# Kernel optimization log

Hardware: AMD Instinct MI355X
Metric: run time of the kernel (lower is better)

The kernel has to match this reference:

```python
import jax, jax.numpy as jnp
import numpy as np

B, N, H, D = 4, 2048, 8, 64
DM = 512  # model dim = H * D


def setup_inputs() -> dict:
    key = jax.random.key(0)
    ks = jax.random.split(key, 8)
    x = jax.random.normal(ks[0], (B, N, DM), dtype=jnp.float32)
    mask_k = jax.random.randint(ks[1], (B, N), 0, 5) > 0
    mask_q = jax.random.randint(ks[2], (B, N), 0, 5) > 0
    s_in = 1.0 / np.sqrt(DM)
    s_out = 1.0 / np.sqrt(H * D)
    Wq = jax.random.normal(ks[3], (DM, H * D), dtype=jnp.float32) * s_in
    Wk = jax.random.normal(ks[4], (DM, H * D), dtype=jnp.float32) * s_in
    Wv = jax.random.normal(ks[5], (DM, H * D), dtype=jnp.float32) * s_in
    Wo = jax.random.normal(ks[6], (H * D, DM), dtype=jnp.float32) * s_out
    bo = jnp.zeros((DM,), dtype=jnp.float32)
    return {"x": x, "Wq": Wq, "Wk": Wk, "Wv": Wv, "Wo": Wo, "bo": bo,
            "mask_k": mask_k, "mask_q": mask_q}


def reference(x, Wq, Wk, Wv, Wo, bo, mask_k, mask_q):
    b, n, _ = x.shape
    # projections (no bias), split into heads: b n (h d) -> b n h d
    q = (x @ Wq).reshape(b, n, H, D)
    k = (x @ Wk).reshape(b, n, H, D)
    v = (x @ Wv).reshape(b, n, H, D)
    scale = D ** (-0.5)
    sim = jnp.einsum('bihd,bjhd->bijh', q, k) * scale  # [b, i, j, h]
    big_neg = jnp.finfo(jnp.float32).min
    sim = jnp.where(mask_k[:, None, :, None], sim, big_neg)
    sim = jnp.where(mask_q[:, :, None, None], sim, big_neg)
    attn = jax.nn.softmax(sim, axis=-2)  # softmax over key axis j
    out = jnp.einsum('bijh,bjhd->bihd', attn, v).reshape(b, n, H * D)
    return out @ Wo + bo
```

## Files before the change

### kernel.cpp

```cpp
#include <hip/hip_runtime.h>

typedef _Float16 f16;
typedef __fp16   fp16x2 __attribute__((ext_vector_type(2)));
typedef _Float16 f16x8 __attribute__((ext_vector_type(8)));
typedef float    f32x4 __attribute__((ext_vector_type(4)));

#define MFMA16(A, B, C) __builtin_amdgcn_mfma_f32_16x16x32_f16((A), (B), (C), 0, 0, 0)

__device__ __forceinline__ void gl_lds16(const void* g, void* l) {
  __builtin_amdgcn_global_load_lds(
      (const __attribute__((address_space(1))) void*)g,
      (__attribute__((address_space(3))) void*)l, 16, 0, 0);
}

static constexpr size_t OFF_XH  = 0;
static constexpr size_t OFF_WQT = 8388608;
static constexpr size_t OFF_WOT = OFF_WQT + 3 * 524288;
static constexpr size_t OFF_QH  = OFF_WOT + 524288;
static constexpr size_t OFF_KH  = OFF_QH + 8388608;
static constexpr size_t OFF_VT  = OFF_KH + 8388608;
static constexpr size_t OFF_A2  = OFF_VT + 8388608;
static constexpr size_t OFF_AMK = OFF_A2 + 8388608;
static constexpr size_t OFF_VM  = OFF_AMK + 32768;

#define QSCALE 0.18033688011112042f
#define NEGFIX -11.541560327111708f

__global__ void k_cvt_x(const float* __restrict__ x, f16* __restrict__ xh,
                        const int* __restrict__ mask_k, float* __restrict__ amk) {
  int i = blockIdx.x * blockDim.x + threadIdx.x;
  const float4* p = (const float4*)x + (size_t)i * 2;
  float4 a = p[0], b = p[1];
  f16x8 o = { (f16)a.x, (f16)a.y, (f16)a.z, (f16)a.w,
              (f16)b.x, (f16)b.y, (f16)b.z, (f16)b.w };
  *((f16x8*)xh + i) = o;
  if (i < 8192) amk[i] = mask_k[i] ? 0.0f : -1000.0f;
}

__global__ void k_cvt_w4(const float* __restrict__ w0, const float* __restrict__ w1,
                         const float* __restrict__ w2, const float* __restrict__ w3,
                         f16* __restrict__ dst) {
  __shared__ float tile[32][33];
  const int z = blockIdx.z;
  const float* w = (z == 0) ? w0 : (z == 1) ? w1 : (z == 2) ? w2 : w3;
  const float sc = (z == 0) ? QSCALE : 1.0f;
  f16* wt = dst + (size_t)z * 262144;
  int tx = threadIdx.x & 31, ty = threadIdx.x >> 5;
  int bx = blockIdx.x, by = blockIdx.y;
#pragma unroll
  for (int i = 0; i < 32; i += 8)
    tile[ty + i][tx] = w[(size_t)(by * 32 + ty + i) * 512 + bx * 32 + tx];
  __syncthreads();
#pragma unroll
  for (int i = 0; i < 32; i += 8)
    wt[(size_t)(bx * 32 + ty + i) * 512 + by * 32 + tx] = (f16)(tile[tx][ty + i] * sc);
}

__global__ void k_vmean(const f16* __restrict__ Vt, float* __restrict__ vm) {
  int row = blockIdx.x * 4 + (threadIdx.x >> 6);
  int lane = threadIdx.x & 63;
  const f16x8* p = (const f16x8*)(Vt + (size_t)row * 2048) + lane;
  float s = 0.f;
#pragma unroll
  for (int i = 0; i < 4; ++i) {
    f16x8 v = p[i * 64];
#pragma unroll
    for (int e = 0; e < 8; ++e) s += (float)v[e];
  }
#pragma unroll
  for (int i = 32; i; i >>= 1) s += __shfl_xor(s, i, 64);
  if (lane == 0) vm[row] = s * (1.0f / 2048.0f);
}

template <int MODE, int BM, int BN>
__global__ __launch_bounds__(256, (MODE == 2 ? 3 : 2))
void k_gemm(const f16* __restrict__ A, const f16* __restrict__ Bt,
            void* __restrict__ O0, void* __restrict__ O1, void* __restrict__ O2,
            const float* __restrict__ bias) {
  constexpr int MR = BM / 32, NF = BN / 32;
  constexpr int AP = BM / 32, BP = BN / 32;
  constexpr int ABYTES = BM * 128;
  constexpr int BBYTES = BN * 128;
  constexpr int SM_STAGE  = 2 * (ABYTES + BBYTES);
  constexpr int SM_BOUNCE = (MODE == 3) ? 128 * 136 * 2 : 0;
  constexpr int SM = SM_STAGE > SM_BOUNCE ? SM_STAGE : SM_BOUNCE;
  __shared__ __align__(16) char smem[SM];
  const int t = threadIdx.x;
  const int lane = t & 63, w = t >> 6;
  const int wr = w >> 1, wc = w & 1;
  const int l15 = lane & 15, l4 = lane >> 4;
  const int lr = lane >> 3, lc = lane & 7;
  const int flat = blockIdx.x + gridDim.x * blockIdx.y;
  const int nwg  = gridDim.x * gridDim.y;
  const int sw   = (flat & 7) * (nwg >> 3) + (flat >> 3);
  const int row0 = (sw / gridDim.x) * BM;
  const int col0 = (sw % gridDim.x) * BN;

  f32x4 acc[MR][NF] = {};

  auto stage = [&](int kt, int buf) {
    char* dA = smem + buf * ABYTES + w * 1024;
    char* dB = smem + 2 * ABYTES + buf * BBYTES + w * 1024;
#pragma unroll
    for (int p = 0; p < AP; ++p) {
      int r = p * 32 + w * 8 + lr;
      gl_lds16((const char*)A + ((size_t)(row0 + r) * 512 + kt) * 2 + ((lc ^ (r & 7)) << 4),
               dA + p * 4096);
    }
#pragma unroll
    for (int p = 0; p < BP; ++p) {
      int r = p * 32 + w * 8 + lr;
      gl_lds16((const char*)Bt + ((size_t)(col0 + r) * 512 + kt) * 2 + ((lc ^ (r & 7)) << 4),
               dB + p * 4096);
    }
  };

  stage(0, 0);
  for (int ks = 0; ks < 8; ++ks) {
    const int buf = ks & 1;
    __syncthreads();
    if (ks < 7) stage((ks + 1) * 64, buf ^ 1);
    const char* cA = smem + buf * ABYTES;
    const char* cB = smem + 2 * ABYTES + buf * BBYTES;
    __builtin_amdgcn_s_setprio(1);
#pragma unroll
    for (int kb = 0; kb < 2; ++kb) {
      f16x8 af[MR], bf[NF];
#pragma unroll
      for (int m = 0; m < MR; ++m) {
        int r = wr * (BM / 2) + m * 16 + l15;
        int lb = r * 128 + kb * 64 + l4 * 16;
        af[m] = *(const f16x8*)(cA + (lb ^ ((r & 7) << 4)));
      }
#pragma unroll
      for (int n = 0; n < NF; ++n) {
        int r = wc * (BN / 2) + n * 16 + l15;
        int lb = r * 128 + kb * 64 + l4 * 16;
        bf[n] = *(const f16x8*)(cB + (lb ^ ((r & 7) << 4)));
      }
#pragma unroll
      for (int m = 0; m < MR; ++m)
#pragma unroll
        for (int n = 0; n < NF; ++n)
          acc[m][n] = MFMA16(af[m], bf[n], acc[m][n]);
    }
    __builtin_amdgcn_s_setprio(0);
  }

  if (MODE == 2) {
#pragma unroll
    for (int m = 0; m < MR; ++m)
#pragma unroll
      for (int n = 0; n < NF; ++n) {
        int gr = row0 + wr * (BM / 2) + m * 16 + l4 * 4;
        int gc = col0 + wc * (BN / 2) + n * 16 + l15;
        float* C = (float*)O0;
        float bv = bias[gc];
#pragma unroll
        for (int rr = 0; rr < 4; ++rr)
          C[(size_t)(gr + rr) * 512 + gc] = acc[m][n][rr] + bv;
      }
  } else {
    int seg = col0 >> 9;
    if (seg < 2) {
      __syncthreads();
      f16* bb = (f16*)smem;
#pragma unroll
      for (int m = 0; m < MR; ++m)
#pragma unroll
        for (int n = 0; n < NF; ++n) {
          int r = wr * (BM / 2) + m * 16 + l4 * 4;
          int c = wc * (BN / 2) + n * 16 + l15;
#pragma unroll
          for (int rr = 0; rr < 4; ++rr)
            bb[(r + rr) * 136 + c] = (f16)acc[m][n][rr];
        }
      __syncthreads();
      f16* C = (f16*)(seg == 0 ? O0 : O1);
      int cbase = col0 & 511;
#pragma unroll
      for (int i = 0; i < 8; ++i) {
        int idx = i * 256 + t;
        int r = idx >> 4, c8 = (idx & 15) * 8;
        uint4 v = *(const uint4*)(bb + r * 136 + c8);
        *(uint4*)(C + (size_t)(row0 + r) * 512 + cbase + c8) = v;
      }
    } else {
#pragma unroll
      for (int m = 0; m < MR; ++m)
#pragma unroll
        for (int n = 0; n < NF; ++n) {
          int gr = row0 + wr * (BM / 2) + m * 16 + l4 * 4;
          int lcol = (col0 & 511) + wc * (BN / 2) + n * 16 + l15;
          f16* C = (f16*)O2;
          int hh = lcol >> 6, dd = lcol & 63;
          int bb2 = gr >> 11, ns = gr & 2047;
          union { uint2 u2; f16 v[4]; } pk;
#pragma unroll
          for (int rr = 0; rr < 4; ++rr) pk.v[rr] = (f16)acc[m][n][rr];
          *(uint2*)(C + (size_t)((bb2 * 8 + hh) * 64 + dd) * 2048 + ns) = pk.u2;
        }
    }
  }
}

__global__ __launch_bounds__(256, 3)
void k_attn(const f16* __restrict__ Q, const f16* __restrict__ K,
            const f16* __restrict__ Vt, const float* __restrict__ amk,
            const int* __restrict__ mask_q, const float* __restrict__ vmean,
            f16* __restrict__ A2) {
  __shared__ __align__(16) f16 sK[2][64 * 64];
  __shared__ __align__(16) f16 sV[2][64 * 64];
  __shared__ __align__(16) f16 sP[4][32 * 64];
  const int t = threadIdx.x, lane = t & 63, w = t >> 6;
  const int l15 = lane & 15, l4 = lane >> 4;
  const int lr = lane >> 3, lc = lane & 7;
  const int sw = (blockIdx.x & 7) * 64 + (blockIdx.x >> 3);
  const int qx = sw & 15, bh = sw >> 4;
  const int b = bh >> 3, h = bh & 7;
  const int q0 = qx * 128 + w * 32;

  f16x8 qa[2][2];
#pragma unroll
  for (int g = 0; g < 2; ++g) {
    const f16* qb = Q + (size_t)(b * 2048 + q0 + g * 16 + l15) * 512 + h * 64 + l4 * 8;
    qa[g][0] = *(const f16x8*)qb;
    qa[g][1] = *(const f16x8*)(qb + 32);
  }

  const f16x8 onesv = { (f16)1.f, (f16)1.f, (f16)1.f, (f16)1.f,
                        (f16)1.f, (f16)1.f, (f16)1.f, (f16)1.f };
  f32x4 o[2][4] = {};
  f32x4 oex[2] = {};

  const char* Kbase  = (const char*)K + ((size_t)b * 2048 * 512 + h * 64) * 2;
  const char* VtBase = (const char*)Vt + ((size_t)(b * 8 + h) * 64) * 2048 * 2;
  const float* amkb = amk + b * 2048;
  char* sPw = (char*)&sP[w][0];

  auto stage = [&](int kv, int buf) {
#pragma unroll
    for (int p = 0; p < 2; ++p) {
      int r = p * 32 + w * 8 + lr;
      gl_lds16(Kbase + (size_t)(kv + r) * 1024 + ((lc ^ (r & 7)) << 4),
               (char*)&sK[buf][0] + p * 4096 + w * 1024);
    }
#pragma unroll
    for (int p = 0; p < 2; ++p) {
      int d = p * 32 + w * 8 + lr;
      gl_lds16(VtBase + ((size_t)d * 2048 + kv) * 2 + ((lc ^ (d & 7)) << 4),
               (char*)&sV[buf][0] + p * 4096 + w * 1024);
    }
  };

  stage(0, 0);
  for (int it = 0; it < 32; ++it) {
    const int kv = it * 64, buf = it & 1;
    __syncthreads();
    if (it < 31) stage(kv + 64, buf ^ 1);
    const char* cK = (const char*)&sK[buf][0];
    const char* cV = (const char*)&sV[buf][0];

    f32x4 amv[4];
#pragma unroll
    for (int jf = 0; jf < 4; ++jf)
      amv[jf] = *(const f32x4*)(amkb + kv + jf * 16 + l4 * 4);

    f32x4 sT[2][4];
    __builtin_amdgcn_s_setprio(1);
#pragma unroll
    for (int jf = 0; jf < 4; ++jf) {
      int r = jf * 16 + l15;
      int base = r * 128 + l4 * 16;
      f16x8 k0 = *(const f16x8*)(cK + (base ^ ((r & 7) << 4)));
      f16x8 k1 = *(const f16x8*)(cK + ((base + 64) ^ ((r & 7) << 4)));
#pragma unroll
      for (int g = 0; g < 2; ++g) {
        f32x4 z = { NEGFIX, NEGFIX, NEGFIX, NEGFIX };
        z = MFMA16(k0, qa[g][0], z);
        z = MFMA16(k1, qa[g][1], z);
        sT[g][jf] = z;
      }
    }
    __builtin_amdgcn_s_setprio(0);

#pragma unroll
    for (int g = 0; g < 2; ++g)
#pragma unroll
      for (int jf = 0; jf < 4; ++jf) {
        float p0 = __builtin_amdgcn_exp2f(sT[g][jf][0] + amv[jf][0]);
        float p1 = __builtin_amdgcn_exp2f(sT[g][jf][1] + amv[jf][1]);
        float p2 = __builtin_amdgcn_exp2f(sT[g][jf][2] + amv[jf][2]);
        float p3 = __builtin_amdgcn_exp2f(sT[g][jf][3] + amv[jf][3]);
        fp16x2 a01 = __builtin_amdgcn_cvt_pkrtz(p0, p1);
        fp16x2 a23 = __builtin_amdgcn_cvt_pkrtz(p2, p3);
        uint2 pk = { __builtin_bit_cast(unsigned, a01),
                     __builtin_bit_cast(unsigned, a23) };
        int row = g * 16 + l15;
        int boff = row * 128 + jf * 32 + l4 * 8;
        *(uint2*)(sPw + (boff ^ ((row & 7) << 4))) = pk;
      }

    __builtin_amdgcn_s_setprio(1);
#pragma unroll
    for (int kb = 0; kb < 2; ++kb) {
      f16x8 pa[2];
#pragma unroll
      for (int g = 0; g < 2; ++g) {
        int rq = g * 16 + l15;
        int pbase = rq * 128 + kb * 64 + l4 * 16;
        pa[g] = *(const f16x8*)(sPw + (pbase ^ ((rq & 7) << 4)));
        oex[g] = MFMA16(pa[g], onesv, oex[g]);
      }
#pragma unroll
      for (int df = 0; df < 4; ++df) {
        int d = df * 16 + l15;
        int vbase = d * 128 + kb * 64 + l4 * 16;
        f16x8 bv = *(const f16x8*)(cV + (vbase ^ ((d & 7) << 4)));
#pragma unroll
        for (int g = 0; g < 2; ++g)
          o[g][df] = MFMA16(pa[g], bv, o[g][df]);
      }
    }
    __builtin_amdgcn_s_setprio(0);
  }

#pragma unroll
  for (int g = 0; g < 2; ++g) {
    const int4 mq4 = *(const int4*)(mask_q + b * 2048 + q0 + g * 16 + l4 * 4);
    const int mq[4] = { mq4.x, mq4.y, mq4.z, mq4.w };
    float inv[4];
#pragma unroll
    for (int rr = 0; rr < 4; ++rr) inv[rr] = 1.0f / oex[g][rr];
#pragma unroll
    for (int df = 0; df < 4; ++df) {
      float vm = vmean[(b * 8 + h) * 64 + df * 16 + l15];
#pragma unroll
      for (int rr = 0; rr < 4; ++rr) {
        float val = mq[rr] ? (o[g][df][rr] * inv[rr]) : vm;
        A2[(size_t)(b * 2048 + q0 + g * 16 + l4 * 4 + rr) * 512 + h * 64 + df * 16 + l15] =
            (f16)val;
      }
    }
  }
}

extern "C" void kernel_launch(void* const* d_in, const int* in_sizes, int n_in,
                              void* d_out, int out_size, void* d_ws, size_t ws_size,
                              hipStream_t stream) {
  (void)in_sizes; (void)n_in; (void)out_size; (void)ws_size;
  const float* x   = (const float*)d_in[0];
  const float* Wq  = (const float*)d_in[1];
  const float* Wk  = (const float*)d_in[2];
  const float* Wv  = (const float*)d_in[3];
  const float* Wo  = (const float*)d_in[4];
  const float* bo  = (const float*)d_in[5];
  const int* mask_k = (const int*)d_in[6];
  const int* mask_q = (const int*)d_in[7];
  float* out = (float*)d_out;
  char* ws = (char*)d_ws;

  f16* Xh   = (f16*)(ws + OFF_XH);
  f16* Wqkv = (f16*)(ws + OFF_WQT);
  f16* Wot  = (f16*)(ws + OFF_WOT);
  f16* Qh   = (f16*)(ws + OFF_QH);
  f16* Kh   = (f16*)(ws + OFF_KH);
  f16* Vt   = (f16*)(ws + OFF_VT);
  f16* A2   = (f16*)(ws + OFF_A2);
  float* AMK = (float*)(ws + OFF_AMK);
  float* VM  = (float*)(ws + OFF_VM);

  k_cvt_x<<<2048, 256, 0, stream>>>(x, Xh, mask_k, AMK);
  k_cvt_w4<<<dim3(16, 16, 4), 256, 0, stream>>>(Wq, Wk, Wv, Wo, Wqkv);

  k_gemm<3, 128, 128><<<dim3(12, 64), 256, 0, stream>>>(Xh, Wqkv, Qh, Kh, Vt, nullptr);

  k_vmean<<<512, 256, 0, stream>>>(Vt, VM);

  k_attn<<<512, 256, 0, stream>>>(Qh, Kh, Vt, AMK, mask_q, VM, A2);

  k_gemm<2, 128, 64><<<dim3(8, 64), 256, 0, stream>>>(A2, Wot, out, nullptr, nullptr, bo);
}
```

Baseline: 169.3 us.

## Halve per-block query tile in attention and narrow QKV GEMM tile for occupancy

Measured after the change: 176.0 us. +3.9%, slower.

```diff
diff --git a/kernel.cpp b/kernel.cpp
--- a/kernel.cpp
+++ b/kernel.cpp
@@ -73,7 +73,7 @@
 }
 
 template <int MODE, int BM, int BN>
-__global__ __launch_bounds__(256, (MODE == 2 ? 3 : 2))
+__global__ __launch_bounds__(256, 3)
 void k_gemm(const f16* __restrict__ A, const f16* __restrict__ Bt,
             void* __restrict__ O0, void* __restrict__ O1, void* __restrict__ O2,
             const float* __restrict__ bias) {
@@ -82,7 +82,7 @@
   constexpr int ABYTES = BM * 128;
   constexpr int BBYTES = BN * 128;
   constexpr int SM_STAGE  = 2 * (ABYTES + BBYTES);
-  constexpr int SM_BOUNCE = (MODE == 3) ? 128 * 136 * 2 : 0;
+  constexpr int SM_BOUNCE = (MODE == 3) ? 128 * (BN + 8) * 2 : 0;
   constexpr int SM = SM_STAGE > SM_BOUNCE ? SM_STAGE : SM_BOUNCE;
   __shared__ __align__(16) char smem[SM];
   const int t = threadIdx.x;
@@ -161,6 +161,8 @@
           C[(size_t)(gr + rr) * 512 + gc] = acc[m][n][rr] + bv;
       }
   } else {
+    constexpr int BSTR = BN + 8;
+    constexpr int RB = BN / 8;
     int seg = col0 >> 9;
     if (seg < 2) {
       __syncthreads();
@@ -173,16 +175,16 @@
           int c = wc * (BN / 2) + n * 16 + l15;
 #pragma unroll
           for (int rr = 0; rr < 4; ++rr)
-            bb[(r + rr) * 136 + c] = (f16)acc[m][n][rr];
+            bb[(r + rr) * BSTR + c] = (f16)acc[m][n][rr];
         }
       __syncthreads();
       f16* C = (f16*)(seg == 0 ? O0 : O1);
       int cbase = col0 & 511;
 #pragma unroll
-      for (int i = 0; i < 8; ++i) {
+      for (int i = 0; i < (128 * RB) / 256; ++i) {
         int idx = i * 256 + t;
-        int r = idx >> 4, c8 = (idx & 15) * 8;
-        uint4 v = *(const uint4*)(bb + r * 136 + c8);
+        int r = idx / RB, c8 = (idx % RB) * 8;
+        uint4 v = *(const uint4*)(bb + r * BSTR + c8);
         *(uint4*)(C + (size_t)(row0 + r) * 512 + cbase + c8) = v;
       }
     } else {
@@ -204,34 +206,33 @@
   }
 }
 
-__global__ __launch_bounds__(256, 3)
+__global__ __launch_bounds__(256, 4)
 void k_attn(const f16* __restrict__ Q, const f16* __restrict__ K,
             const f16* __restrict__ Vt, const float* __restrict__ amk,
             const int* __restrict__ mask_q, const float* __restrict__ vmean,
             f16* __restrict__ A2) {
   __shared__ __align__(16) f16 sK[2][64 * 64];
   __shared__ __align__(16) f16 sV[2][64 * 64];
-  __shared__ __align__(16) f16 sP[4][32 * 64];
+  __shared__ __align__(16) f16 sP[4][16 * 64];
   const int t = threadIdx.x, lane = t & 63, w = t >> 6;
   const int l15 = lane & 15, l4 = lane >> 4;
   const int lr = lane >> 3, lc = lane & 7;
-  const int sw = (blockIdx.x & 7) * 64 + (blockIdx.x >> 3);
-  const int qx = sw & 15, bh = sw >> 4;
+  const int sw = (blockIdx.x & 7) * 128 + (blockIdx.x >> 3);
+  const int qx = sw & 31, bh = sw >> 5;
   const int b = bh >> 3, h = bh & 7;
-  const int q0 = qx * 128 + w * 32;
-
-  f16x8 qa[2][2];
-#pragma unroll
-  for (int g = 0; g < 2; ++g) {
-    const f16* qb = Q + (size_t)(b * 2048 + q0 + g * 16 + l15) * 512 + h * 64 + l4 * 8;
-    qa[g][0] = *(const f16x8*)qb;
-    qa[g][1] = *(const f16x8*)(qb + 32);
+  const int q0 = qx * 64 + w * 16;
+
+  f16x8 qa[2];
+  {
+    const f16* qb = Q + (size_t)(b * 2048 + q0 + l15) * 512 + h * 64 + l4 * 8;
+    qa[0] = *(const f16x8*)qb;
+    qa[1] = *(const f16x8*)(qb + 32);
   }
 
   const f16x8 onesv = { (f16)1.f, (f16)1.f, (f16)1.f, (f16)1.f,
                         (f16)1.f, (f16)1.f, (f16)1.f, (f16)1.f };
-  f32x4 o[2][4] = {};
-  f32x4 oex[2] = {};
+  f32x4 o[4] = {};
+  f32x4 oex = {};
 
   const char* Kbase  = (const char*)K + ((size_t)b * 2048 * 512 + h * 64) * 2;
   const char* VtBase = (const char*)Vt + ((size_t)(b * 8 + h) * 64) * 2048 * 2;
@@ -266,7 +267,7 @@
     for (int jf = 0; jf < 4; ++jf)
       amv[jf] = *(const f32x4*)(amkb + kv + jf * 16 + l4 * 4);
 
-    f32x4 sT[2][4];
+    f32x4 sT[4];
     __builtin_amdgcn_s_setprio(1);
 #pragma unroll
     for (int jf = 0; jf < 4; ++jf) {
@@ -274,73 +275,58 @@
       int base = r * 128 + l4 * 16;
       f16x8 k0 = *(const f16x8*)(cK + (base ^ ((r & 7) << 4)));
       f16x8 k1 = *(const f16x8*)(cK + ((base + 64) ^ ((r & 7) << 4)));
-#pragma unroll
-      for (int g = 0; g < 2; ++g) {
-        f32x4 z = { NEGFIX, NEGFIX, NEGFIX, NEGFIX };
-        z = MFMA16(k0, qa[g][0], z);
-        z = MFMA16(k1, qa[g][1], z);
-        sT[g][jf] = z;
-      }
+      f32x4 z = { NEGFIX, NEGFIX, NEGFIX, NEGFIX };
+      z = MFMA16(k0, qa[0], z);
+      z = MFMA16(k1, qa[1], z);
+      sT[jf] = z;
     }
     __builtin_amdgcn_s_setprio(0);
 
 #pragma unroll
-    for (int g = 0; g < 2; ++g)
-#pragma unroll
-      for (int jf = 0; jf < 4; ++jf) {
-        float p0 = __builtin_amdgcn_exp2f(sT[g][jf][0] + amv[jf][0]);
-        float p1 = __builtin_amdgcn_exp2f(sT[g][jf][1] + amv[jf][1]);
-        float p2 = __builtin_amdgcn_exp2f(sT[g][jf][2] + amv[jf][2]);
-        float p3 = __builtin_amdgcn_exp2f(sT[g][jf][3] + amv[jf][3]);
-        fp16x2 a01 = __builtin_amdgcn_cvt_pkrtz(p0, p1);
-        fp16x2 a23 = __builtin_amdgcn_cvt_pkrtz(p2, p3);
-        uint2 pk = { __builtin_bit_cast(unsigned, a01),
-                     __builtin_bit_cast(unsigned, a23) };
-        int row = g * 16 + l15;
-        int boff = row * 128 + jf * 32 + l4 * 8;
-        *(uint2*)(sPw + (boff ^ ((row & 7) << 4))) = pk;
-      }
+    for (int jf = 0; jf < 4; ++jf) {
+      float p0 = __builtin_amdgcn_exp2f(sT[jf][0] + amv[jf][0]);
+      float p1 = __builtin_amdgcn_exp2f(sT[jf][1] + amv[jf][1]);
+      float p2 = __builtin_amdgcn_exp2f(sT[jf][2] + amv[jf][2]);
+      float p3 = __builtin_amdgcn_exp2f(sT[jf][3] + amv[jf][3]);
+      fp16x2 a01 = __builtin_amdgcn_cvt_pkrtz(p0, p1);
+      fp16x2 a23 = __builtin_amdgcn_cvt_pkrtz(p2, p3);
+      uint2 pk = { __builtin_bit_cast(unsigned, a01),
+                   __builtin_bit_cast(unsigned, a23) };
+      int row = l15;
+      int boff = row * 128 + jf * 32 + l4 * 8;
+      *(uint2*)(sPw + (boff ^ ((row & 7) << 4))) = pk;
+    }
 
     __builtin_amdgcn_s_setprio(1);
 #pragma unroll
     for (int kb = 0; kb < 2; ++kb) {
-      f16x8 pa[2];
-#pragma unroll
-      for (int g = 0; g < 2; ++g) {
-        int rq = g * 16 + l15;
-        int pbase = rq * 128 + kb * 64 + l4 * 16;
-        pa[g] = *(const f16x8*)(sPw + (pbase ^ ((rq & 7) << 4)));
-        oex[g] = MFMA16(pa[g], onesv, oex[g]);
-      }
+      int pbase = l15 * 128 + kb * 64 + l4 * 16;
+      f16x8 pa = *(const f16x8*)(sPw + (pbase ^ ((l15 & 7) << 4)));
+      oex = MFMA16(pa, onesv, oex);
 #pragma unroll
       for (int df = 0; df < 4; ++df) {
         int d = df * 16 + l15;
         int vbase = d * 128 + kb * 64 + l4 * 16;
         f16x8 bv = *(const f16x8*)(cV + (vbase ^ ((d & 7) << 4)));
-#pragma unroll
-        for (int g = 0; g < 2; ++g)
-          o[g][df] = MFMA16(pa[g], bv, o[g][df]);
+        o[df] = MFMA16(pa, bv, o[df]);
       }
     }
     __builtin_amdgcn_s_setprio(0);
   }
 
-#pragma unroll
-  for (int g = 0; g < 2; ++g) {
-    const int4 mq4 = *(const int4*)(mask_q + b * 2048 + q0 + g * 16 + l4 * 4);
-    const int mq[4] = { mq4.x, mq4.y, mq4.z, mq4.w };
-    float inv[4];
-#pragma unroll
-    for (int rr = 0; rr < 4; ++rr) inv[rr] = 1.0f / oex[g][rr];
-#pragma unroll
-    for (int df = 0; df < 4; ++df) {
-      float vm = vmean[(b * 8 + h) * 64 + df * 16 + l15];
-#pragma unroll
-      for (int rr = 0; rr < 4; ++rr) {
-        float val = mq[rr] ? (o[g][df][rr] * inv[rr]) : vm;
-        A2[(size_t)(b * 2048 + q0 + g * 16 + l4 * 4 + rr) * 512 + h * 64 + df * 16 + l15] =
-            (f16)val;
-      }
+  const int4 mq4 = *(const int4*)(mask_q + b * 2048 + q0 + l4 * 4);
+  const int mq[4] = { mq4.x, mq4.y, mq4.z, mq4.w };
+  float inv[4];
+#pragma unroll
+  for (int rr = 0; rr < 4; ++rr) inv[rr] = 1.0f / oex[rr];
+#pragma unroll
+  for (int df = 0; df < 4; ++df) {
+    float vm = vmean[(b * 8 + h) * 64 + df * 16 + l15];
+#pragma unroll
+    for (int rr = 0; rr < 4; ++rr) {
+      float val = mq[rr] ? (o[df][rr] * inv[rr]) : vm;
+      A2[(size_t)(b * 2048 + q0 + l4 * 4 + rr) * 512 + h * 64 + df * 16 + l15] =
+          (f16)val;
     }
   }
 }
@@ -373,11 +359,11 @@
   k_cvt_x<<<2048, 256, 0, stream>>>(x, Xh, mask_k, AMK);
   k_cvt_w4<<<dim3(16, 16, 4), 256, 0, stream>>>(Wq, Wk, Wv, Wo, Wqkv);
 
-  k_gemm<3, 128, 128><<<dim3(12, 64), 256, 0, stream>>>(Xh, Wqkv, Qh, Kh, Vt, nullptr);
+  k_gemm<3, 128, 64><<<dim3(24, 64), 256, 0, stream>>>(Xh, Wqkv, Qh, Kh, Vt, nullptr);
 
   k_vmean<<<512, 256, 0, stream>>>(Vt, VM);
 
-  k_attn<<<512, 256, 0, stream>>>(Qh, Kh, Vt, AMK, mask_q, VM, A2);
+  k_attn<<<1024, 256, 0, stream>>>(Qh, Kh, Vt, AMK, mask_q, VM, A2);
 
   k_gemm<2, 128, 64><<<dim3(8, 64), 256, 0, stream>>>(A2, Wot, out, nullptr, nullptr, bo);
 }
```
